# Kernel optimization log

Hardware: AMD Instinct MI355X
Metric: run time of the kernel (lower is better)

## Reference

```python
import jax, jax.numpy as jnp
import numpy as np

N_NODES = 50000
N_EDGES = 800000
NODE_DIM = 64
HIDDEN = 128
OUT_DIM = 256
N_LAYERS = 3


def setup_inputs() -> dict:
    key = jax.random.key(0)
    ks = jax.random.split(key, 12)
    inp = {
        'x': jax.random.normal(ks[0], (N_NODES, NODE_DIM), dtype=jnp.float32),
        'src': jax.random.randint(ks[1], (N_EDGES,), 0, N_NODES, dtype=jnp.int32),
        'dst': jax.random.randint(ks[2], (N_EDGES,), 0, N_NODES, dtype=jnp.int32),
        'Wp': jax.random.normal(ks[3], (NODE_DIM, HIDDEN), dtype=jnp.float32) / np.sqrt(NODE_DIM),
        'bp': jax.random.normal(ks[4], (HIDDEN,), dtype=jnp.float32) * 0.01,
        'Wg': jax.random.normal(ks[5], (N_LAYERS, HIDDEN, HIDDEN), dtype=jnp.float32) / np.sqrt(HIDDEN),
        'bg': jax.random.normal(ks[6], (N_LAYERS, HIDDEN), dtype=jnp.float32) * 0.01,
        'W1': jax.random.normal(ks[7], (HIDDEN, HIDDEN), dtype=jnp.float32) / np.sqrt(HIDDEN),
        'b1': jax.random.normal(ks[8], (HIDDEN,), dtype=jnp.float32) * 0.01,
        'W2': jax.random.normal(ks[9], (HIDDEN, OUT_DIM), dtype=jnp.float32) / np.sqrt(HIDDEN),
        'b2': jax.random.normal(ks[10], (OUT_DIM,), dtype=jnp.float32) * 0.01,
    }
    return inp


def reference(x, src, dst, Wp, bp, Wg, bg, W1, b1, W2, b2):
    n = x.shape[0]
    # node_proj
    h = x @ Wp + bp  # [N, H]
    # in-degree per dst node; zero-degree nodes keep a zero message
    deg = jax.ops.segment_sum(jnp.ones_like(src, dtype=h.dtype), dst, num_segments=n)  # [N]
    inv_deg = jnp.where(deg > 0, 1.0 / jnp.maximum(deg, 1.0), 0.0)[:, None]  # [N,1]
    for l in range(Wg.shape[0]):
        # gather neighbor embeddings along edges, mean-aggregate into dst
        msg = jax.ops.segment_sum(h[src], dst, num_segments=n) * inv_deg  # [N, H]
        h = jax.nn.relu(h + msg @ Wg[l] + bg[l])
    g = jnp.mean(h, axis=0)  # [H]
    latent = jax.nn.relu(g @ W1 + b1) @ W2 + b2  # [OUT_DIM]
    return latent
```

## Files before the change

kernel.cpp:

```cpp
#include <hip/hip_runtime.h>
#include <hip/hip_fp16.h>

#define H   128
#define ND  64
#define TILE_R 64
#define CAP 64

typedef _Float16 f16x8 __attribute__((ext_vector_type(8)));
typedef float    f32x4 __attribute__((ext_vector_type(4)));

__device__ __forceinline__ unsigned short f2h(float f) {
  return __half_as_ushort(__float2half(f));
}
__device__ __forceinline__ float h2f(unsigned short u) {
  return __half2float(__ushort_as_half(u));
}


__global__ __launch_bounds__(256) void scatter_part_k(
    const int* __restrict__ src, const int* __restrict__ dst,
    int* __restrict__ cnt, unsigned short* __restrict__ ssrc,
    int E, int psz) {
  int grp = blockIdx.x & 7;
  int lo = grp * psz, hi = lo + psz;
  int stride = (gridDim.x >> 3) * 256;
  for (int e = (blockIdx.x >> 3) * 256 + threadIdx.x; e < E; e += stride) {
    int d = dst[e];
    if (d >= lo && d < hi) {
      int p = atomicAdd(&cnt[d], 1);
      if (p < CAP) ssrc[(size_t)d * CAP + p] = (unsigned short)src[e];
    }
  }
}


__global__ __launch_bounds__(256) void prep_all_k(const float* __restrict__ Wg,
                                                  const float* __restrict__ Wp,
                                                  unsigned short* __restrict__ wfrag,
                                                  unsigned short* __restrict__ wpfrag) {
  __shared__ float sW[H * H];
  if (blockIdx.x < 3) {
    const float* W = Wg + (size_t)blockIdx.x * H * H;
    for (int i = threadIdx.x; i < H * H; i += 256) sW[i] = W[i];
    __syncthreads();
    unsigned short* out = wfrag + (size_t)blockIdx.x * 2048 * 8;
    for (int c = threadIdx.x; c < 2048; c += 256) {
      int lane = c & 63, combo = c >> 6;
      int it = combo >> 2, ks = combo & 3;
      int nc = it * 16 + (lane & 15);
      int kb = ks * 32 + (lane >> 4) * 8;
      unsigned short* o = out + (size_t)c * 8;
#pragma unroll
      for (int j = 0; j < 8; ++j) o[j] = f2h(sW[(kb + j) * H + nc]);
    }
  } else {
    for (int i = threadIdx.x; i < ND * H; i += 256) sW[i] = Wp[i];
    __syncthreads();
    for (int c = threadIdx.x; c < 1024; c += 256) {
      int lane = c & 63, combo = c >> 6;
      int it = combo >> 1, ks = combo & 1;
      int nc = it * 16 + (lane & 15);
      int kb = ks * 32 + (lane >> 4) * 8;
      unsigned short* o = wpfrag + (size_t)c * 8;
#pragma unroll
      for (int j = 0; j < 8; ++j) o[j] = f2h(sW[(kb + j) * H + nc]);
    }
  }
}


__global__ __launch_bounds__(256, 4) void proj_mfma_k(const float* __restrict__ x,
                                                      const unsigned short* __restrict__ wpfrag,
                                                      const float* __restrict__ bp,
                                                      unsigned short* __restrict__ hout,
                                                      int n) {
  __shared__ unsigned short sB[1024 * 8];
  uint4* sB4 = (uint4*)sB;
  const uint4* wsrc = (const uint4*)wpfrag;
  for (int i = threadIdx.x; i < 1024; i += 256) sB4[i] = wsrc[i];
  __syncthreads();

  int wave = threadIdx.x >> 6, lane = threadIdx.x & 63;
  int quad = lane >> 4, n16 = lane & 15;
  int node = blockIdx.x * 64 + wave * 16 + n16;

  union { unsigned short s[8]; uint4 u; f16x8 h; } bm[2];
  if (node < n) {
    const float* xr = x + (size_t)node * ND;
#pragma unroll
    for (int ks = 0; ks < 2; ++ks) {
      const float* pk = xr + ks * 32 + quad * 8;
      float4 A0 = *(const float4*)pk;
      float4 A1 = *(const float4*)(pk + 4);
      bm[ks].s[0] = f2h(A0.x); bm[ks].s[1] = f2h(A0.y);
      bm[ks].s[2] = f2h(A0.z); bm[ks].s[3] = f2h(A0.w);
      bm[ks].s[4] = f2h(A1.x); bm[ks].s[5] = f2h(A1.y);
      bm[ks].s[6] = f2h(A1.z); bm[ks].s[7] = f2h(A1.w);
    }
  } else {
    bm[0].u = make_uint4(0, 0, 0, 0);
    bm[1].u = make_uint4(0, 0, 0, 0);
  }

  f32x4 acc[8] = {};
#pragma unroll
  for (int it = 0; it < 8; ++it) {
#pragma unroll
    for (int ks = 0; ks < 2; ++ks) {
      union { uint4 u; f16x8 h; } aw;
      aw.u = sB4[(it * 2 + ks) * 64 + lane];
      acc[it] = __builtin_amdgcn_mfma_f32_16x16x32_f16(aw.h, bm[ks].h, acc[it], 0, 0, 0);
    }
  }

  unsigned short* rout = hout + (size_t)node * H;
#pragma unroll
  for (int it = 0; it < 8; ++it) {
    int f0 = it * 16 + quad * 4;
    float4 bv = *(const float4*)(bp + f0);
    ushort4 o = make_ushort4(f2h(acc[it][0] + bv.x), f2h(acc[it][1] + bv.y),
                             f2h(acc[it][2] + bv.z), f2h(acc[it][3] + bv.w));
    *(ushort4*)(rout + f0) = o;
  }
}


__global__ __launch_bounds__(256) void aggregate_w_k(
    const unsigned short* __restrict__ hin,
    const int* __restrict__ cnt,
    const unsigned short* __restrict__ ssrc,
    unsigned short* __restrict__ msgh, int n) {
  int node = blockIdx.x * 4 + (threadIdx.x >> 6);
  if (node >= n) return;
  int l = threadIdx.x & 63;
  int sub = l >> 4, li = l & 15;
  int deg = cnt[node]; if (deg > CAP) deg = CAP;
  const __half2 z = __floats2half2_rn(0.f, 0.f);
  __half2 acc[4] = {z, z, z, z};
  if (deg > 0) {
    int eid = (int)ssrc[(size_t)node * CAP + (l < deg ? l : 0)];
    int j = 0;
#pragma unroll 4
    for (; j + 4 <= deg; j += 4) {
      int s = __shfl(eid, j + sub, 64);
      union { uint4 u; __half2 h[4]; } v;
      v.u = *(const uint4*)(hin + (size_t)s * H + li * 8);
      acc[0] = __hadd2(acc[0], v.h[0]);
      acc[1] = __hadd2(acc[1], v.h[1]);
      acc[2] = __hadd2(acc[2], v.h[2]);
      acc[3] = __hadd2(acc[3], v.h[3]);
    }
    if (j < deg) {
      int jj = j + sub;
      int s = __shfl(eid, jj < deg ? jj : deg - 1, 64);
      if (jj < deg) {
        union { uint4 u; __half2 h[4]; } v;
        v.u = *(const uint4*)(hin + (size_t)s * H + li * 8);
        acc[0] = __hadd2(acc[0], v.h[0]);
        acc[1] = __hadd2(acc[1], v.h[1]);
        acc[2] = __hadd2(acc[2], v.h[2]);
        acc[3] = __hadd2(acc[3], v.h[3]);
      }
    }
  }
#pragma unroll
  for (int k = 0; k < 4; ++k) {
    union { __half2 h; unsigned int u; } a, b, c;
    a.h = acc[k];
    b.u = __shfl_xor(a.u, 16, 64);
    a.h = __hadd2(a.h, b.h);
    c.u = __shfl_xor(a.u, 32, 64);
    acc[k] = __hadd2(a.h, c.h);
  }
  if (sub == 0) {
    float inv = (deg > 0) ? 1.0f / (float)deg : 0.f;
    uint4 o;
    unsigned int* op = (unsigned int*)&o;
#pragma unroll
    for (int k = 0; k < 4; ++k) {
      float lo = __low2float(acc[k]) * inv;
      float hi = __high2float(acc[k]) * inv;
      op[k] = (unsigned int)f2h(lo) | ((unsigned int)f2h(hi) << 16);
    }
    *(uint4*)(msgh + (size_t)node * H + li * 8) = o;
  }
}


__global__ __launch_bounds__(256, 4) void update_mfma_k(
    const unsigned short* __restrict__ hin,
    unsigned short* __restrict__ hout,
    const unsigned short* __restrict__ msgh,
    const unsigned short* __restrict__ wfrag,
    const float* __restrict__ bg, int n) {
  __shared__ unsigned short sB[2048 * 8];
  uint4* sB4 = (uint4*)sB;
  const uint4* wsrc = (const uint4*)wfrag;
  for (int i = threadIdx.x; i < 2048; i += 256) sB4[i] = wsrc[i];
  __syncthreads();

  int wave = threadIdx.x >> 6, lane = threadIdx.x & 63;
  int quad = lane >> 4, n16 = lane & 15;
  int node = blockIdx.x * 64 + wave * 16 + n16;

  union { uint4 u; f16x8 h; } bm[4];
  const unsigned short* mrow = msgh + (size_t)node * H;
#pragma unroll
  for (int ks = 0; ks < 4; ++ks)
    bm[ks].u = *(const uint4*)(mrow + ks * 32 + quad * 8);

  f32x4 acc[8] = {};
#pragma unroll
  for (int it = 0; it < 8; ++it) {
#pragma unroll
    for (int ks = 0; ks < 4; ++ks) {
      union { uint4 u; f16x8 h; } aw;
      aw.u = sB4[(it * 4 + ks) * 64 + lane];
      acc[it] = __builtin_amdgcn_mfma_f32_16x16x32_f16(aw.h, bm[ks].h, acc[it], 0, 0, 0);
    }
  }

  const unsigned short* rin = hin + (size_t)node * H;
  unsigned short* rout = hout + (size_t)node * H;
#pragma unroll
  for (int it = 0; it < 8; ++it) {
    int f0 = it * 16 + quad * 4;
    float4 bv = *(const float4*)(bg + f0);
    ushort4 old = *(const ushort4*)(rin + f0);
    float v0 = h2f(old.x) + acc[it][0] + bv.x; v0 = v0 > 0.f ? v0 : 0.f;
    float v1 = h2f(old.y) + acc[it][1] + bv.y; v1 = v1 > 0.f ? v1 : 0.f;
    float v2 = h2f(old.z) + acc[it][2] + bv.z; v2 = v2 > 0.f ? v2 : 0.f;
    float v3 = h2f(old.w) + acc[it][3] + bv.w; v3 = v3 > 0.f ? v3 : 0.f;
    *(ushort4*)(rout + f0) = make_ushort4(f2h(v0), f2h(v1), f2h(v2), f2h(v3));
  }
}


__global__ __launch_bounds__(256) void reduce_mean_h_k(const unsigned short* __restrict__ hb,
                                                       float* __restrict__ gsum, int n) {
  int c  = threadIdx.x & 31;
  int rg = threadIdx.x >> 5;
  float4 acc = {0.f, 0.f, 0.f, 0.f};
  for (int row = blockIdx.x * 8 + rg; row < n; row += gridDim.x * 8) {
    ushort4 v = ((const ushort4*)(hb + (size_t)row * H))[c];
    acc.x += h2f(v.x); acc.y += h2f(v.y);
    acc.z += h2f(v.z); acc.w += h2f(v.w);
  }
  __shared__ float4 s[256];
  s[threadIdx.x] = acc;
  __syncthreads();
  if (threadIdx.x < 32) {
    float4 t = s[c];
#pragma unroll
    for (int k = 1; k < 8; ++k) {
      float4 q = s[k * 32 + c];
      t.x += q.x; t.y += q.y; t.z += q.z; t.w += q.w;
    }
    atomicAdd(&gsum[c * 4 + 0], t.x);
    atomicAdd(&gsum[c * 4 + 1], t.y);
    atomicAdd(&gsum[c * 4 + 2], t.z);
    atomicAdd(&gsum[c * 4 + 3], t.w);
  }
}


__global__ __launch_bounds__(256) void mlp_k(const float* __restrict__ gsum,
                                             const float* __restrict__ W1,
                                             const float* __restrict__ b1,
                                             const float* __restrict__ W2,
                                             const float* __restrict__ b2,
                                             float* __restrict__ out, float invN) {
  __shared__ float g[H];
  __shared__ float hid[H];
  int tid = threadIdx.x;
  if (tid < H) g[tid] = gsum[tid] * invN;
  __syncthreads();
  if (tid < H) {
    float acc = b1[tid];
    for (int k = 0; k < H; ++k) acc += g[k] * W1[k * H + tid];
    hid[tid] = acc > 0.f ? acc : 0.f;
  }
  __syncthreads();
  float acc = b2[tid];
  for (int k = 0; k < H; ++k) acc += hid[k] * W2[k * 256 + tid];
  out[tid] = acc;
}


extern "C" void kernel_launch(void* const* d_in, const int* in_sizes, int n_in,
                              void* d_out, int out_size, void* d_ws, size_t ws_size,
                              hipStream_t stream) {
  const float* x  = (const float*)d_in[0];
  const int*   src = (const int*)d_in[1];
  const int*   dst = (const int*)d_in[2];
  const float* Wp = (const float*)d_in[3];
  const float* bp = (const float*)d_in[4];
  const float* Wg = (const float*)d_in[5];
  const float* bg = (const float*)d_in[6];
  const float* W1 = (const float*)d_in[7];
  const float* b1 = (const float*)d_in[8];
  const float* W2 = (const float*)d_in[9];
  const float* b2 = (const float*)d_in[10];
  float* out = (float*)d_out;

  const int N = in_sizes[0] / ND;
  const int E = in_sizes[1];
  const int N_pad = ((N + TILE_R - 1) / TILE_R) * TILE_R;
  const size_t NH = (size_t)N_pad * H;
  const int psz = (N_pad + 7) / 8;

  char* p = (char*)d_ws;
  unsigned short* hb0   = (unsigned short*)p; p += NH * sizeof(unsigned short);
  unsigned short* hb1   = (unsigned short*)p; p += NH * sizeof(unsigned short);
  unsigned short* msgh  = (unsigned short*)p; p += NH * sizeof(unsigned short);
  unsigned short* wfrag = (unsigned short*)p; p += 3 * 2048 * 8 * sizeof(unsigned short);
  unsigned short* wpfrag= (unsigned short*)p; p += 1024 * 8 * sizeof(unsigned short);
  unsigned short* ssrc  = (unsigned short*)p; p += (size_t)N_pad * CAP * sizeof(unsigned short);
  int*   cnt  = (int*)p;   p += (size_t)N_pad * sizeof(int);
  float* gsum = (float*)p; p += H * sizeof(float);

  const int ntiles = N_pad / TILE_R;

  hipMemsetAsync(cnt, 0, ((size_t)N_pad + H) * sizeof(int), stream);

  scatter_part_k<<<2048, 256, 0, stream>>>(src, dst, cnt, ssrc, E, psz);

  prep_all_k<<<4, 256, 0, stream>>>(Wg, Wp, wfrag, wpfrag);

  proj_mfma_k<<<ntiles, 256, 0, stream>>>(x, wpfrag, bp, hb0, N);

  unsigned short* hin = hb0;
  unsigned short* hout = hb1;
  for (int l = 0; l < 3; ++l) {
    aggregate_w_k<<<(N + 3) / 4, 256, 0, stream>>>(hin, cnt, ssrc, msgh, N);
    update_mfma_k<<<ntiles, 256, 0, stream>>>(hin, hout, msgh,
                                              wfrag + (size_t)l * 2048 * 8,
                                              bg + (size_t)l * H, N);
    unsigned short* t = hin; hin = hout; hout = t;
  }

  reduce_mean_h_k<<<256, 256, 0, stream>>>(hin, gsum, N);
  mlp_k<<<1, 256, 0, stream>>>(gsum, W1, b1, W2, b2, out, 1.0f / (float)N);
}
```

Baseline: 297.9 us.

## Fuse launch chain: zeroing into prep, scatter with projection, pool with MLP

Moves the memset of the counters and gsum into extra blocks of the weight-prep kernel. The edge-scatter kernel and the input-projection kernel become one launch with disjoint block ranges, so both run concurrently. The mean-reduction and final MLP are merged using a last-block-done atomic counter. The aim is fewer launches and less serialization between independent stages, at the cost of a threadfence/atomic handshake and mixed-role blocks in one grid.

```diff
diff --git a/kernel.cpp b/kernel.cpp
--- a/kernel.cpp
+++ b/kernel.cpp
@@ -5,6 +5,7 @@
 #define ND  64
 #define TILE_R 64
 #define CAP 64
+#define NSCAT 2048
 
 typedef _Float16 f16x8 __attribute__((ext_vector_type(8)));
 typedef float    f32x4 __attribute__((ext_vector_type(4)));
@@ -14,30 +15,16 @@
 }
 __device__ __forceinline__ float h2f(unsigned short u) {
   return __half2float(__ushort_as_half(u));
-}
-
-
-__global__ __launch_bounds__(256) void scatter_part_k(
-    const int* __restrict__ src, const int* __restrict__ dst,
-    int* __restrict__ cnt, unsigned short* __restrict__ ssrc,
-    int E, int psz) {
-  int grp = blockIdx.x & 7;
-  int lo = grp * psz, hi = lo + psz;
-  int stride = (gridDim.x >> 3) * 256;
-  for (int e = (blockIdx.x >> 3) * 256 + threadIdx.x; e < E; e += stride) {
-    int d = dst[e];
-    if (d >= lo && d < hi) {
-      int p = atomicAdd(&cnt[d], 1);
-      if (p < CAP) ssrc[(size_t)d * CAP + p] = (unsigned short)src[e];
-    }
-  }
 }
 
 
 __global__ __launch_bounds__(256) void prep_all_k(const float* __restrict__ Wg,
                                                   const float* __restrict__ Wp,
                                                   unsigned short* __restrict__ wfrag,
-                                                  unsigned short* __restrict__ wpfrag) {
+                                                  unsigned short* __restrict__ wpfrag,
+                                                  int* __restrict__ cnt, int n_pad,
+                                                  float* __restrict__ gsum,
+                                                  int* __restrict__ done) {
   __shared__ float sW[H * H];
   if (blockIdx.x < 3) {
     const float* W = Wg + (size_t)blockIdx.x * H * H;
@@ -53,7 +40,7 @@
 #pragma unroll
       for (int j = 0; j < 8; ++j) o[j] = f2h(sW[(kb + j) * H + nc]);
     }
-  } else {
+  } else if (blockIdx.x == 3) {
     for (int i = threadIdx.x; i < ND * H; i += 256) sW[i] = Wp[i];
     __syncthreads();
     for (int c = threadIdx.x; c < 1024; c += 256) {
@@ -65,16 +52,39 @@
 #pragma unroll
       for (int j = 0; j < 8; ++j) o[j] = f2h(sW[(kb + j) * H + nc]);
     }
-  }
-}
-
-
-__global__ __launch_bounds__(256, 4) void proj_mfma_k(const float* __restrict__ x,
-                                                      const unsigned short* __restrict__ wpfrag,
-                                                      const float* __restrict__ bp,
-                                                      unsigned short* __restrict__ hout,
-                                                      int n) {
+  } else {
+    int zb = blockIdx.x - 4;
+    int chunk = (n_pad + 15) >> 4;
+    int lo = zb * chunk, hi = lo + chunk; if (hi > n_pad) hi = n_pad;
+    for (int i = lo + threadIdx.x; i < hi; i += 256) cnt[i] = 0;
+    if (zb == 0) {
+      if (threadIdx.x < H) gsum[threadIdx.x] = 0.f;
+      if (threadIdx.x == 0) *done = 0;
+    }
+  }
+}
+
+
+__global__ __launch_bounds__(256) void scatter_proj_k(
+    const int* __restrict__ src, const int* __restrict__ dst,
+    int* __restrict__ cnt, unsigned short* __restrict__ ssrc, int E, int psz,
+    const float* __restrict__ x, const unsigned short* __restrict__ wpfrag,
+    const float* __restrict__ bp, unsigned short* __restrict__ hout, int n) {
   __shared__ unsigned short sB[1024 * 8];
+  if ((int)blockIdx.x < NSCAT) {
+    int grp = blockIdx.x & 7;
+    int lo = grp * psz, hi = lo + psz;
+    int stride = (NSCAT >> 3) * 256;
+    for (int e = ((int)blockIdx.x >> 3) * 256 + (int)threadIdx.x; e < E; e += stride) {
+      int d = dst[e];
+      if (d >= lo && d < hi) {
+        int p = atomicAdd(&cnt[d], 1);
+        if (p < CAP) ssrc[(size_t)d * CAP + p] = (unsigned short)src[e];
+      }
+    }
+    return;
+  }
+
   uint4* sB4 = (uint4*)sB;
   const uint4* wsrc = (const uint4*)wpfrag;
   for (int i = threadIdx.x; i < 1024; i += 256) sB4[i] = wsrc[i];
@@ -82,7 +92,7 @@
 
   int wave = threadIdx.x >> 6, lane = threadIdx.x & 63;
   int quad = lane >> 4, n16 = lane & 15;
-  int node = blockIdx.x * 64 + wave * 16 + n16;
+  int node = ((int)blockIdx.x - NSCAT) * 64 + wave * 16 + n16;
 
   union { unsigned short s[8]; uint4 u; f16x8 h; } bm[2];
   if (node < n) {
@@ -236,8 +246,12 @@
 }
 
 
-__global__ __launch_bounds__(256) void reduce_mean_h_k(const unsigned short* __restrict__ hb,
-                                                       float* __restrict__ gsum, int n) {
+__global__ __launch_bounds__(256) void pool_mlp_k(
+    const unsigned short* __restrict__ hb, float* __restrict__ gsum,
+    int* __restrict__ done,
+    const float* __restrict__ W1, const float* __restrict__ b1,
+    const float* __restrict__ W2, const float* __restrict__ b2,
+    float* __restrict__ out, float invN, int n, int nblocks) {
   int c  = threadIdx.x & 31;
   int rg = threadIdx.x >> 5;
   float4 acc = {0.f, 0.f, 0.f, 0.f};
@@ -261,29 +275,28 @@
     atomicAdd(&gsum[c * 4 + 2], t.z);
     atomicAdd(&gsum[c * 4 + 3], t.w);
   }
-}
-
-
-__global__ __launch_bounds__(256) void mlp_k(const float* __restrict__ gsum,
-                                             const float* __restrict__ W1,
-                                             const float* __restrict__ b1,
-                                             const float* __restrict__ W2,
-                                             const float* __restrict__ b2,
-                                             float* __restrict__ out, float invN) {
+  __threadfence();
+  __syncthreads();
+  __shared__ int lastflag;
+  if (threadIdx.x == 0)
+    lastflag = (atomicAdd(done, 1) == nblocks - 1) ? 1 : 0;
+  __syncthreads();
+  if (!lastflag) return;
+
   __shared__ float g[H];
   __shared__ float hid[H];
   int tid = threadIdx.x;
-  if (tid < H) g[tid] = gsum[tid] * invN;
+  if (tid < H) g[tid] = atomicAdd(&gsum[tid], 0.0f) * invN;
   __syncthreads();
   if (tid < H) {
-    float acc = b1[tid];
-    for (int k = 0; k < H; ++k) acc += g[k] * W1[k * H + tid];
-    hid[tid] = acc > 0.f ? acc : 0.f;
-  }
-  __syncthreads();
-  float acc = b2[tid];
-  for (int k = 0; k < H; ++k) acc += hid[k] * W2[k * 256 + tid];
-  out[tid] = acc;
+    float a = b1[tid];
+    for (int k = 0; k < H; ++k) a += g[k] * W1[k * H + tid];
+    hid[tid] = a > 0.f ? a : 0.f;
+  }
+  __syncthreads();
+  float a = b2[tid];
+  for (int k = 0; k < H; ++k) a += hid[k] * W2[k * 256 + tid];
+  out[tid] = a;
 }
 
 
@@ -318,16 +331,15 @@
   unsigned short* ssrc  = (unsigned short*)p; p += (size_t)N_pad * CAP * sizeof(unsigned short);
   int*   cnt  = (int*)p;   p += (size_t)N_pad * sizeof(int);
   float* gsum = (float*)p; p += H * sizeof(float);
+  int*   done = (int*)p;   p += sizeof(int);
 
   const int ntiles = N_pad / TILE_R;
-
-  hipMemsetAsync(cnt, 0, ((size_t)N_pad + H) * sizeof(int), stream);
-
-  scatter_part_k<<<2048, 256, 0, stream>>>(src, dst, cnt, ssrc, E, psz);
-
-  prep_all_k<<<4, 256, 0, stream>>>(Wg, Wp, wfrag, wpfrag);
-
-  proj_mfma_k<<<ntiles, 256, 0, stream>>>(x, wpfrag, bp, hb0, N);
+  const int POOLB = 256;
+
+  prep_all_k<<<20, 256, 0, stream>>>(Wg, Wp, wfrag, wpfrag, cnt, N_pad, gsum, done);
+
+  scatter_proj_k<<<NSCAT + ntiles, 256, 0, stream>>>(src, dst, cnt, ssrc, E, psz,
+                                                     x, wpfrag, bp, hb0, N);
 
   unsigned short* hin = hb0;
   unsigned short* hout = hb1;
@@ -339,6 +351,6 @@
     unsigned short* t = hin; hin = hout; hout = t;
   }
 
-  reduce_mean_h_k<<<256, 256, 0, stream>>>(hin, gsum, N);
-  mlp_k<<<1, 256, 0, stream>>>(gsum, W1, b1, W2, b2, out, 1.0f / (float)N);
-}
+  pool_mlp_k<<<POOLB, 256, 0, stream>>>(hin, gsum, done, W1, b1, W2, b2, out,
+                                        1.0f / (float)N, N, POOLB);
+}
```

New measurement: 294.4 us. No clear change (-1.2%).
